# Kernel optimization log

Hardware: AMD Instinct MI355X
Metric: run time of the kernel (lower is better)

## Reference

```python
import jax, jax.numpy as jnp
import numpy as np

NW, NT = 200000, 100000
DW, DT = 128, 64
HID, HEADS, OUT = 64, 2, 2
HC = HID * HEADS  # 128
E = 500000
NEG_SLOPE = 0.2


def setup_inputs() -> dict:
    key = jax.random.key(0)
    ks = iter(jax.random.split(key, 40))

    def nrm(shape, scale):
        return jax.random.normal(next(ks), shape, dtype=jnp.float32) * scale

    inp = {
        "x_wallet": nrm((NW, DW), 1.0),
        "x_token": nrm((NT, DT), 1.0),
        # per-node-type input projections Linear(in, hidden)
        "lin_w_W": nrm((DW, HID), 1.0 / np.sqrt(DW)),
        "lin_w_b": jnp.zeros((HID,), jnp.float32),
        "lin_t_W": nrm((DT, HID), 1.0 / np.sqrt(DT)),
        "lin_t_b": jnp.zeros((HID,), jnp.float32),
        # GAT layer 0: in=HID(64) -> H*C(128), stacked over 3 edge types
        "Wsrc0": nrm((3, HID, HC), 1.0 / np.sqrt(HID)),
        "Wdst0": nrm((3, HID, HC), 1.0 / np.sqrt(HID)),
        "atts0": nrm((3, HEADS, HID), 1.0 / np.sqrt(HID)),
        "attd0": nrm((3, HEADS, HID), 1.0 / np.sqrt(HID)),
        "b0": jnp.zeros((3, HC), jnp.float32),
        # GAT layer 1: in=H*C(128) -> H*C(128)
        "Wsrc1": nrm((3, HC, HC), 1.0 / np.sqrt(HC)),
        "Wdst1": nrm((3, HC, HC), 1.0 / np.sqrt(HC)),
        "atts1": nrm((3, HEADS, HID), 1.0 / np.sqrt(HID)),
        "attd1": nrm((3, HEADS, HID), 1.0 / np.sqrt(HID)),
        "b1": jnp.zeros((3, HC), jnp.float32),
        # classifiers Linear(H*C, out)
        "cls_w_W": nrm((HC, OUT), 1.0 / np.sqrt(HC)),
        "cls_w_b": jnp.zeros((OUT,), jnp.float32),
        "cls_t_W": nrm((HC, OUT), 1.0 / np.sqrt(HC)),
        "cls_t_b": jnp.zeros((OUT,), jnp.float32),
        # edge indices: [2, E] with row0 = src ids, row1 = dst ids
        "e_wt": jnp.stack([jax.random.randint(next(ks), (E,), 0, NW),
                            jax.random.randint(next(ks), (E,), 0, NT)]).astype(jnp.int64),
        "e_tw": jnp.stack([jax.random.randint(next(ks), (E,), 0, NT),
                            jax.random.randint(next(ks), (E,), 0, NW)]).astype(jnp.int64),
        "e_ww": jnp.stack([jax.random.randint(next(ks), (E,), 0, NW),
                            jax.random.randint(next(ks), (E,), 0, NW)]).astype(jnp.int64),
    }
    return inp


def gat_conv(x_src, x_dst, edge, Wsrc, Wdst, att_s, att_d, bias, n_dst):
    # bipartite GATConv: project, per-edge attention, segment softmax over dst, scatter-sum
    hs = (x_src @ Wsrc).reshape(-1, HEADS, HID)  # [Ns,H,C]
    hd = (x_dst @ Wdst).reshape(-1, HEADS, HID)  # [Nd,H,C]
    a_s = jnp.einsum("nhc,hc->nh", hs, att_s)    # [Ns,H]
    a_d = jnp.einsum("nhc,hc->nh", hd, att_d)    # [Nd,H]
    s, d = edge[0], edge[1]
    alpha = jax.nn.leaky_relu(a_s[s] + a_d[d], NEG_SLOPE)  # [E,H]
    m = jax.ops.segment_max(alpha, d, num_segments=n_dst)
    m = jnp.where(jnp.isfinite(m), m, 0.0)  # nodes with no in-edges
    ex = jnp.exp(alpha - m[d])
    den = jax.ops.segment_sum(ex, d, num_segments=n_dst)
    alpha = ex / (den[d] + 1e-16)
    out = jax.ops.segment_sum(alpha[:, :, None] * hs[s], d, num_segments=n_dst)  # [Nd,H,C]
    return out.reshape(n_dst, HC) + bias


def reference(x_wallet, x_token, lin_w_W, lin_w_b, lin_t_W, lin_t_b,
              Wsrc0, Wdst0, atts0, attd0, b0,
              Wsrc1, Wdst1, atts1, attd1, b1,
              cls_w_W, cls_w_b, cls_t_W, cls_t_b,
              e_wt, e_tw, e_ww):
    xw = x_wallet @ lin_w_W + lin_w_b
    xt = x_token @ lin_t_W + lin_t_b
    for Wsrc, Wdst, ats, atd, b in ((Wsrc0, Wdst0, atts0, attd0, b0),
                                     (Wsrc1, Wdst1, atts1, attd1, b1)):
        # edge type 0: wallet->token, 1: token->wallet, 2: wallet->wallet; HeteroConv aggr='sum'
        out_t = gat_conv(xw, xt, e_wt, Wsrc[0], Wdst[0], ats[0], atd[0], b[0], NT)
        out_w = (gat_conv(xt, xw, e_tw, Wsrc[1], Wdst[1], ats[1], atd[1], b[1], NW)
                 + gat_conv(xw, xw, e_ww, Wsrc[2], Wdst[2], ats[2], atd[2], b[2], NW))
        xw = jax.nn.elu(out_w)
        xt = jax.nn.elu(out_t)
    logits_w = xw @ cls_w_W + cls_w_b  # [NW,2]
    logits_t = xt @ cls_t_W + cls_t_b  # [NT,2]
    return jnp.concatenate([logits_w, logits_t], axis=0)  # [NW+NT,2]
```

## Files before the change

kernel.cpp:

```cpp
#include <hip/hip_runtime.h>
#include <stdint.h>

typedef unsigned short ushort_t;
typedef short s8v __attribute__((ext_vector_type(8)));
typedef float f4v __attribute__((ext_vector_type(4)));

#define NW 200000
#define NT 100000
#define EE 500000
#define NSEG (NT + NW + NW)

__device__ __forceinline__ float b2f(unsigned short u){
  union { unsigned int i; float f; } v; v.i = ((unsigned int)u) << 16; return v.f;
}
__device__ __forceinline__ unsigned short f2b(float f){
  unsigned int x = __float_as_uint(f);
  unsigned int r = x + 0x7fffu + ((x >> 16) & 1u);
  return (unsigned short)(r >> 16);
}
__device__ __forceinline__ float ldf(const void* p, long idx, int fm){
  return fm ? ((const float*)p)[idx] : b2f(((const ushort_t*)p)[idx]);
}

__global__ void detect_kern(const int* ewt, const int* etw, const int* eww,
                            const unsigned* xw_words, int* mode){
  if (threadIdx.x == 0 && blockIdx.x == 0){
    unsigned o = 0;
    for (int i = 0; i < 64; ++i)
      o |= (unsigned)ewt[2 * i + 1] | (unsigned)etw[2 * i + 1] | (unsigned)eww[2 * i + 1];
    mode[0] = (o == 0) ? 1 : 0;
    int viol = 0;
    for (int i = 0; i < 256; ++i){
      unsigned s = xw_words[i] & 0xffffu;
      unsigned e = (s >> 7) & 0xffu;
      if (!(s == 0u || s == 0x8000u || (e >= 90u && e <= 140u))) viol++;
    }
    mode[1] = (viol > 8) ? 1 : 0;
  }
}

struct TDesc { const void* src; ushort_t* dst; long ebase; int K; int N; };
struct TDesc8 { TDesc d[8]; };
__global__ void transpose8(TDesc8 td, const int* mode){
  int fm = mode[1];
  int mi = blockIdx.x >> 6;
  TDesc t = td.d[mi];
  int e = ((blockIdx.x & 63) << 8) + threadIdx.x;
  if (e < t.K * t.N){
    int k = e / t.N, n = e - k * t.N;
    t.dst[n * t.K + k] = f2b(ldf(t.src, t.ebase + e, fm));
  }
}

__global__ void uprep(const void* Wsrc0, const void* Wdst0, const void* atts0, const void* attd0,
                      const void* Wsrc1, const void* Wdst1, const void* atts1, const void* attd1,
                      float* Uw0, float* Ut0, float* Uw1, float* Ut1, const int* mode){
  int fm = mode[1];
  int id = blockIdx.x * 256 + threadIdx.x;
  if (id >= (64 + 128) * 12) return;
  int layer = (id >= 64 * 12);
  int rem = layer ? id - 64 * 12 : id;
  int K = layer ? 128 : 64;
  int k = rem / 12, j = rem % 12;
  const void* Ws = layer ? Wsrc1 : Wsrc0;
  const void* Wd = layer ? Wdst1 : Wdst0;
  const void* As = layer ? atts1 : atts0;
  const void* Ad = layer ? attd1 : attd0;
  int t, h; bool src;
  if (j < 8){ const int tt[8] = {0,0,2,2,1,1,2,2}; t = tt[j]; h = j & 1; src = (j < 4); }
  else { int jj = j - 8; t = (jj < 2) ? 1 : 0; h = jj & 1; src = (jj < 2); }
  const void* W = src ? Ws : Wd;
  const void* A = src ? As : Ad;
  float acc = 0.f;
  for (int c = 0; c < 64; ++c)
    acc += ldf(W, (long)(t * K + k) * 128 + h * 64 + c, fm) * ldf(A, t * 128 + h * 64 + c, fm);
  if (j < 8) (layer ? Uw1 : Uw0)[k * 8 + j] = acc;
  else       (layer ? Ut1 : Ut0)[k * 4 + (j - 8)] = acc;
}

__global__ void hist_kern(const int* ewt, const int* etw, const int* eww, const int* mode, int* deg){
  int i = blockIdx.x * 256 + threadIdx.x;
  if (i >= 3 * EE) return;
  int md = mode[0];
  int t = i / EE, e = i - t * EE;
  const int* ep = (t == 0) ? ewt : (t == 1) ? etw : eww;
  int d = md ? ep[2 * (EE + e)] : ep[EE + e];
  int base = (t == 0) ? 0 : (t == 1) ? NT : NT + NW;
  atomicAdd(&deg[base + d], 1);
}

__global__ __launch_bounds__(512) void scan1(const int* deg, int* excl, int* sums){
  __shared__ int pair[512];
  int t = threadIdx.x;
  int base = blockIdx.x * 1024;
  int i0 = base + 2 * t;
  int a = (i0 < NSEG) ? deg[i0] : 0;
  int b = (i0 + 1 < NSEG) ? deg[i0 + 1] : 0;
  int ps = a + b;
  pair[t] = ps;
  __syncthreads();
  for (int off = 1; off < 512; off <<= 1){
    int v = (t >= off) ? pair[t - off] : 0;
    __syncthreads();
    if (t >= off) pair[t] += v;
    __syncthreads();
  }
  int epair = pair[t] - ps;
  if (i0 < NSEG) excl[i0] = epair;
  if (i0 + 1 < NSEG) excl[i0 + 1] = epair + a;
  if (t == 511) sums[blockIdx.x] = pair[511];
}

__global__ __launch_bounds__(512) void scan2(int* sums, int nch){
  __shared__ int s[512];
  int t = threadIdx.x;
  int orig = (t < nch) ? sums[t] : 0;
  s[t] = orig;
  __syncthreads();
  for (int off = 1; off < 512; off <<= 1){
    int v = (t >= off) ? s[t - off] : 0;
    __syncthreads();
    if (t >= off) s[t] += v;
    __syncthreads();
  }
  if (t < nch) sums[t] = s[t] - orig;
}

__global__ void scan3(int* rowptr, int* cursor, const int* sums){
  int i = blockIdx.x * 256 + threadIdx.x;
  if (i < NSEG){
    int v = rowptr[i] + sums[i >> 10];
    rowptr[i] = v; cursor[i] = v;
  }
  if (i == 0) rowptr[NSEG] = 3 * EE;
}

__global__ void fill_kern(const int* ewt, const int* etw, const int* eww, const int* mode,
                          int* cursor, int* adj){
  int i = blockIdx.x * 256 + threadIdx.x;
  if (i >= 3 * EE) return;
  int md = mode[0];
  int t = i / EE, e = i - t * EE;
  const int* ep = (t == 0) ? ewt : (t == 1) ? etw : eww;
  int s = md ? ep[2 * e] : ep[e];
  int d = md ? ep[2 * (EE + e)] : ep[EE + e];
  int base = (t == 0) ? 0 : (t == 1) ? NT : NT + NW;
  int pos = atomicAdd(&cursor[base + d], 1);
  adj[pos] = s;
}

template<int K, int NC, int RS, bool BIAS, bool EXTA>
__global__ __launch_bounds__(256, 2) void gemm_kern(const void* __restrict__ A, const ushort_t* __restrict__ Bt,
    const void* __restrict__ bias, ushort_t* __restrict__ C, int M,
    const int* __restrict__ mode, int nchunk){
  constexpr int CT = NC / 16, KK = K / 32;
  int fm = EXTA ? mode[1] : 0;
  int tid = threadIdx.x, lane = tid & 63, wave = tid >> 6;
  int rl = lane & 15, kq = (lane >> 4) * 8;
  s8v bfrag[CT][KK];
#pragma unroll
  for (int ct = 0; ct < CT; ++ct)
#pragma unroll
    for (int kk = 0; kk < KK; ++kk)
      bfrag[ct][kk] = *(const s8v*)(Bt + (long)(ct * 16 + rl) * K + kk * 32 + kq);
  float biasv[CT];
  if (BIAS){
#pragma unroll
    for (int ct = 0; ct < CT; ++ct) biasv[ct] = ldf(bias, ct * 16 + rl, fm);
  }
  for (int chunk = blockIdx.x; chunk < nchunk; chunk += gridDim.x){
    long m0 = (long)chunk * 128 + wave * 32;
    f4v acc[2][CT];
#pragma unroll
    for (int rt = 0; rt < 2; ++rt)
#pragma unroll
      for (int ct = 0; ct < CT; ++ct) acc[rt][ct] = (f4v){0.f, 0.f, 0.f, 0.f};
#pragma unroll
    for (int rt = 0; rt < 2; ++rt){
      long row = m0 + rt * 16 + rl;
      bool ok = row < (long)M;
#pragma unroll
      for (int kk = 0; kk < KK; ++kk){
        s8v a = (s8v){0,0,0,0,0,0,0,0};
        if (ok){
          long e = row * K + kk * 32 + kq;
          if (EXTA && fm){
            const float* p = (const float*)A + e;
            uint4 lo = *(const uint4*)p;
            uint4 hi = *(const uint4*)(p + 4);
            union { s8v v; unsigned u[4]; } t;
            t.u[0] = (unsigned)f2b(__uint_as_float(lo.x)) | ((unsigned)f2b(__uint_as_float(lo.y)) << 16);
            t.u[1] = (unsigned)f2b(__uint_as_float(lo.z)) | ((unsigned)f2b(__uint_as_float(lo.w)) << 16);
            t.u[2] = (unsigned)f2b(__uint_as_float(hi.x)) | ((unsigned)f2b(__uint_as_float(hi.y)) << 16);
            t.u[3] = (unsigned)f2b(__uint_as_float(hi.z)) | ((unsigned)f2b(__uint_as_float(hi.w)) << 16);
            a = t.v;
          } else {
            a = *(const s8v*)((const ushort_t*)A + e);
          }
        }
#pragma unroll
        for (int ct = 0; ct < CT; ++ct)
          acc[rt][ct] = __builtin_amdgcn_mfma_f32_16x16x32_bf16(a, bfrag[ct][kk], acc[rt][ct], 0, 0, 0);
      }
    }
#pragma unroll
    for (int rt = 0; rt < 2; ++rt){
      long rbase = (long)chunk * 128 + wave * 32 + rt * 16 + (lane >> 4) * 4;
#pragma unroll
      for (int ct = 0; ct < CT; ++ct){
#pragma unroll
        for (int r = 0; r < 4; ++r){
          long gm = rbase + r;
          if (gm < (long)M){
            float v = acc[rt][ct][r];
            if (BIAS) v += biasv[ct];
            C[gm * RS + ct * 16 + rl] = f2b(v);
          }
        }
      }
    }
  }
}

template<int K, bool WAL>
__global__ __launch_bounds__(256) void a_kern(const ushort_t* __restrict__ x, const float* __restrict__ U,
    float* __restrict__ dpq, float* __restrict__ spqA, float* __restrict__ spqB, int N){
  constexpr int NCOL = WAL ? 8 : 4;
  int n = blockIdx.x * 256 + threadIdx.x;
  if (n >= N) return;
  float acc[NCOL];
#pragma unroll
  for (int j = 0; j < NCOL; ++j) acc[j] = 0.f;
  const ushort_t* xr = x + (long)n * K;
#pragma unroll
  for (int k8 = 0; k8 < K / 8; ++k8){
    uint4 v = *(const uint4*)(xr + k8 * 8);
    unsigned uu[4] = {v.x, v.y, v.z, v.w};
#pragma unroll
    for (int i = 0; i < 4; ++i){
      float f0 = b2f((unsigned short)(uu[i] & 0xffffu));
      float f1 = b2f((unsigned short)(uu[i] >> 16));
      const float* Ur = U + (k8 * 8 + i * 2) * NCOL;
#pragma unroll
      for (int j = 0; j < NCOL; ++j) acc[j] += f0 * Ur[j] + f1 * Ur[NCOL + j];
    }
  }
  if (WAL){
    f4v tA = {__expf(acc[0]), __expf(0.2f * acc[0]), __expf(acc[1]), __expf(0.2f * acc[1])};
    *(f4v*)(spqA + (long)n * 4) = tA;
    f4v tB = {__expf(acc[2]), __expf(0.2f * acc[2]), __expf(acc[3]), __expf(0.2f * acc[3])};
    *(f4v*)(spqB + (long)n * 4) = tB;
    f4v d1 = {__expf(acc[4]), __expf(0.2f * acc[4]), __expf(acc[5]), __expf(0.2f * acc[5])};
    f4v d2 = {__expf(acc[6]), __expf(0.2f * acc[6]), __expf(acc[7]), __expf(0.2f * acc[7])};
    *(f4v*)(dpq + (long)n * 8) = d1;
    *(f4v*)(dpq + (long)n * 8 + 4) = d2;
  } else {
    f4v tA = {__expf(acc[0]), __expf(0.2f * acc[0]), __expf(acc[1]), __expf(0.2f * acc[1])};
    *(f4v*)(spqA + (long)n * 4) = tA;
    f4v d0 = {__expf(acc[2]), __expf(0.2f * acc[2]), __expf(acc[3]), __expf(0.2f * acc[3])};
    *(f4v*)(dpq + (long)n * 4) = d0;
  }
}

__device__ __forceinline__ void round_load(const int* __restrict__ adj, int j, int cnt,
    const ushort_t* __restrict__ hs, const float* __restrict__ spq, int c0, int hh,
    float2 (&pq)[8], unsigned (&h)[8]){
#pragma unroll
  for (int i = 0; i < 8; ++i){
    if (i < cnt){
      int s = adj[j + i];
      pq[i] = *(const float2*)(spq + s * 4 + hh * 2);
      h[i] = *(const unsigned*)(hs + (long)s * 128 + c0);
    }
  }
}

__device__ __forceinline__ void round_acc(int cnt, float pd, float qd,
    const float2 (&pq)[8], const unsigned (&h)[8], float& n0, float& n1, float& den){
#pragma unroll
  for (int i = 0; i < 8; ++i){
    if (i < cnt){
      float t = pq[i].x * pd, u = pq[i].y * qd;
      float w = t > 1.f ? t : u;
      den += w;
      n0 += w * b2f((unsigned short)(h[i] & 0xffffu));
      n1 += w * b2f((unsigned short)(h[i] >> 16));
    }
  }
}

__device__ __forceinline__ void classify_store(float o0, float o1, const void* W, const void* b,
    int lane, long g, void* dout, int fm){
  float w00 = ldf(W, 4 * lane + 0, fm), w01 = ldf(W, 4 * lane + 1, fm);
  float w10 = ldf(W, 4 * lane + 2, fm), w11 = ldf(W, 4 * lane + 3, fm);
  float p0 = o0 * w00 + o1 * w10;
  float p1 = o0 * w01 + o1 * w11;
#pragma unroll
  for (int off = 32; off > 0; off >>= 1){ p0 += __shfl_xor(p0, off, 64); p1 += __shfl_xor(p1, off, 64); }
  if (lane == 0){
    float r0 = p0 + ldf(b, 0, fm);
    float r1 = p1 + ldf(b, 1, fm);
    if (fm){ ((float*)dout)[g * 2] = r0; ((float*)dout)[g * 2 + 1] = r1; }
    else { ((ushort_t*)dout)[g * 2] = f2b(r0); ((ushort_t*)dout)[g * 2 + 1] = f2b(r1); }
  }
}

template<bool FINAL>
__global__ __launch_bounds__(256) void agg_tok(const int* __restrict__ rowptr, const int* __restrict__ adj,
    const float* __restrict__ atd, const float* __restrict__ spq0, const ushort_t* __restrict__ hs0,
    const void* __restrict__ bsrc, ushort_t* __restrict__ xt_out,
    const void* __restrict__ clsWt, const void* __restrict__ clsbt,
    void* __restrict__ dout, const int* __restrict__ mode){
  int fm = mode[1];
  int wv = __builtin_amdgcn_readfirstlane(threadIdx.x >> 6);
  int lane = threadIdx.x & 63;
  int hh = lane >> 5, c0 = lane << 1;
  int d = blockIdx.x * 4 + wv;
  float2 dq = *(const float2*)(atd + (long)d * 4 + hh * 2);
  int beg = rowptr[d], end = rowptr[d + 1];
  float n0 = 0.f, n1 = 0.f, den = 0.f;
  for (int j = beg; j < end; j += 8){
    int cnt = min(end - j, 8);
    float2 pq[8]; unsigned h[8];
    round_load(adj, j, cnt, hs0, spq0, c0, hh, pq, h);
    round_acc(cnt, dq.x, dq.y, pq, h, n0, n1, den);
  }
  float inv = 1.f / (den + 1e-16f);
  float o0 = n0 * inv + ldf(bsrc, c0, fm);
  float o1 = n1 * inv + ldf(bsrc, c0 + 1, fm);
  o0 = o0 > 0.f ? o0 : __expf(o0) - 1.f;
  o1 = o1 > 0.f ? o1 : __expf(o1) - 1.f;
  if (!FINAL){
    unsigned pack = (unsigned)f2b(o0) | ((unsigned)f2b(o1) << 16);
    *(unsigned*)(xt_out + (long)d * 128 + c0) = pack;
  } else {
    classify_store(o0, o1, clsWt, clsbt, lane, (long)NW + d, dout, fm);
  }
}

template<bool FINAL>
__global__ __launch_bounds__(256) void agg_wal(const int* __restrict__ rowptr, const int* __restrict__ adj,
    const float* __restrict__ awd, const float* __restrict__ spq1, const float* __restrict__ spq2,
    const ushort_t* __restrict__ hs1, const ushort_t* __restrict__ hs2,
    const void* __restrict__ bsrc, ushort_t* __restrict__ xw_out,
    const void* __restrict__ clsWw, const void* __restrict__ clsbw,
    void* __restrict__ dout, const int* __restrict__ mode){
  int fm = mode[1];
  int wv = __builtin_amdgcn_readfirstlane(threadIdx.x >> 6);
  int lane = threadIdx.x & 63;
  int hh = lane >> 5, c0 = lane << 1;
  int d = blockIdx.x * 4 + wv;
  float2 dq1 = *(const float2*)(awd + (long)d * 8 + hh * 2);
  float2 dq2 = *(const float2*)(awd + (long)d * 8 + 4 + hh * 2);
  int s1 = NT + d, s2 = NT + NW + d;
  int b1 = rowptr[s1], e1 = rowptr[s1 + 1];
  int b2 = rowptr[s2], e2 = rowptr[s2 + 1];
  int c1 = min(e1 - b1, 8), c2 = min(e2 - b2, 8);
  float n10 = 0.f, n11 = 0.f, den1 = 0.f;
  float n20 = 0.f, n21 = 0.f, den2 = 0.f;
  {
    float2 pq1[8], pq2[8]; unsigned h1[8], h2[8];
    if (c1 > 0) round_load(adj, b1, c1, hs1, spq1, c0, hh, pq1, h1);
    if (c2 > 0) round_load(adj, b2, c2, hs2, spq2, c0, hh, pq2, h2);
    if (c1 > 0) round_acc(c1, dq1.x, dq1.y, pq1, h1, n10, n11, den1);
    if (c2 > 0) round_acc(c2, dq2.x, dq2.y, pq2, h2, n20, n21, den2);
  }
  for (int j = b1 + 8; j < e1; j += 8){
    int cnt = min(e1 - j, 8);
    float2 pq[8]; unsigned h[8];
    round_load(adj, j, cnt, hs1, spq1, c0, hh, pq, h);
    round_acc(cnt, dq1.x, dq1.y, pq, h, n10, n11, den1);
  }
  for (int j = b2 + 8; j < e2; j += 8){
    int cnt = min(e2 - j, 8);
    float2 pq[8]; unsigned h[8];
    round_load(adj, j, cnt, hs2, spq2, c0, hh, pq, h);
    round_acc(cnt, dq2.x, dq2.y, pq, h, n20, n21, den2);
  }
  float i1v = 1.f / (den1 + 1e-16f), i2v = 1.f / (den2 + 1e-16f);
  float o0 = n10 * i1v + n20 * i2v + ldf(bsrc, 128 + c0, fm)     + ldf(bsrc, 256 + c0, fm);
  float o1 = n11 * i1v + n21 * i2v + ldf(bsrc, 128 + c0 + 1, fm) + ldf(bsrc, 256 + c0 + 1, fm);
  o0 = o0 > 0.f ? o0 : __expf(o0) - 1.f;
  o1 = o1 > 0.f ? o1 : __expf(o1) - 1.f;
  if (!FINAL){
    unsigned pack = (unsigned)f2b(o0) | ((unsigned)f2b(o1) << 16);
    *(unsigned*)(xw_out + (long)d * 128 + c0) = pack;
  } else {
    classify_store(o0, o1, clsWw, clsbw, lane, (long)d, dout, fm);
  }
}

extern "C" void kernel_launch(void* const* d_in, const int* in_sizes, int n_in,
                              void* d_out, int out_size, void* d_ws, size_t ws_size,
                              hipStream_t stream){
  const void* x_wallet = d_in[0];
  const void* x_token  = d_in[1];
  const void* lin_w_W  = d_in[2];
  const void* lin_w_b  = d_in[3];
  const void* lin_t_W  = d_in[4];
  const void* lin_t_b  = d_in[5];
  const void* Wsrc0    = d_in[6];
  const void* Wdst0    = d_in[7];
  const void* atts0    = d_in[8];
  const void* attd0    = d_in[9];
  const void* b0       = d_in[10];
  const void* Wsrc1    = d_in[11];
  const void* Wdst1    = d_in[12];
  const void* atts1    = d_in[13];
  const void* attd1    = d_in[14];
  const void* b1       = d_in[15];
  const void* cls_w_W  = d_in[16];
  const void* cls_w_b  = d_in[17];
  const void* cls_t_W  = d_in[18];
  const void* cls_t_b  = d_in[19];
  const int* e_wt = (const int*)d_in[20];
  const int* e_tw = (const int*)d_in[21];
  const int* e_ww = (const int*)d_in[22];

  char* ws = (char*)d_ws;
  size_t off = 0;
  auto alloc = [&](size_t bytes) -> char* {
    char* p = ws + off; off += (bytes + 255) & ~(size_t)255; return p;
  };
  int* rowptr = (int*)alloc((size_t)(NSEG + 1) * 4);
  int* deg    = (int*)alloc((size_t)(NSEG + 1) * 4);
  int* adj    = (int*)alloc((size_t)3 * EE * 4);
  int* sums   = (int*)alloc(512 * 4);
  int* mode   = (int*)alloc(8);
  ushort_t* BtLw = (ushort_t*)alloc(64 * 128 * 2);
  ushort_t* BtLt = (ushort_t*)alloc(64 * 64 * 2);
  ushort_t* BtS0 = (ushort_t*)alloc(3 * 128 * 64 * 2);
  ushort_t* BtS1 = (ushort_t*)alloc(3 * 128 * 128 * 2);
  float* Uw0 = (float*)alloc(64 * 8 * 4);
  float* Ut0 = (float*)alloc(64 * 4 * 4);
  float* Uw1 = (float*)alloc(128 * 8 * 4);
  float* Ut1 = (float*)alloc(128 * 4 * 4);
  float* awd = (float*)alloc((size_t)NW * 8 * 4);
  float* atd = (float*)alloc((size_t)NT * 4 * 4);
  float* spq0 = (float*)alloc((size_t)NW * 4 * 4);
  float* spq1 = (float*)alloc((size_t)NT * 4 * 4);
  float* spq2 = (float*)alloc((size_t)NW * 4 * 4);
  ushort_t* hs0 = (ushort_t*)alloc((size_t)NW * 128 * 2);
  ushort_t* hs1 = (ushort_t*)alloc((size_t)NT * 128 * 2);
  ushort_t* hs2 = (ushort_t*)alloc((size_t)NW * 128 * 2);
  ushort_t* xbuf = (ushort_t*)alloc(((size_t)NW + NT) * 128 * 2);
  ushort_t* xw0 = xbuf;
  ushort_t* xt0 = xbuf + (size_t)NW * 64;
  ushort_t* xwB = xbuf;
  ushort_t* xtB = xbuf + (size_t)NW * 128;
  (void)in_sizes; (void)n_in;

  if (off > ws_size){
    hipMemsetAsync(d_out, 0, (size_t)out_size * 2, stream);
    return;
  }

  hipMemsetAsync(deg, 0, (size_t)NSEG * 4, stream);
  detect_kern<<<1, 64, 0, stream>>>(e_wt, e_tw, e_ww, (const unsigned*)x_wallet, mode);

  TDesc8 td;
  td.d[0] = { lin_w_W, BtLw, 0, 128, 64 };
  td.d[1] = { lin_t_W, BtLt, 0, 64, 64 };
  for (int t = 0; t < 3; ++t){
    td.d[2 + t] = { Wsrc0, BtS0 + t * 128 * 64,  (long)t * 64 * 128,  64,  128 };
    td.d[5 + t] = { Wsrc1, BtS1 + t * 128 * 128, (long)t * 128 * 128, 128, 128 };
  }
  transpose8<<<512, 256, 0, stream>>>(td, mode);
  uprep<<<9, 256, 0, stream>>>(Wsrc0, Wdst0, atts0, attd0, Wsrc1, Wdst1, atts1, attd1, Uw0, Ut0, Uw1, Ut1, mode);

  int egrid = (3 * EE + 255) / 256;
  hist_kern<<<egrid, 256, 0, stream>>>(e_wt, e_tw, e_ww, mode, deg);
  int nch = (NSEG + 1023) / 1024;
  scan1<<<nch, 512, 0, stream>>>(deg, rowptr, sums);
  scan2<<<1, 512, 0, stream>>>(sums, nch);
  scan3<<<(NSEG + 255) / 256, 256, 0, stream>>>(rowptr, deg, sums);
  fill_kern<<<egrid, 256, 0, stream>>>(e_wt, e_tw, e_ww, mode, deg, adj);

  const int G = 512;
  int ncW = (NW + 127) / 128, ncT = (NT + 127) / 128;
  int tgrid = NT / 4, wgrid = NW / 4;

  gemm_kern<128, 64, 64, true, true><<<G, 256, 0, stream>>>(x_wallet, BtLw, lin_w_b, xw0, NW, mode, ncW);
  gemm_kern<64, 64, 64, true, true><<<G, 256, 0, stream>>>(x_token, BtLt, lin_t_b, xt0, NT, mode, ncT);

  a_kern<64, true><<<(NW + 255) / 256, 256, 0, stream>>>(xw0, Uw0, awd, spq0, spq2, NW);
  a_kern<64, false><<<(NT + 255) / 256, 256, 0, stream>>>(xt0, Ut0, atd, spq1, nullptr, NT);
  gemm_kern<64, 128, 128, false, false><<<G, 256, 0, stream>>>(xw0, BtS0, nullptr, hs0, NW, mode, ncW);
  agg_tok<false><<<tgrid, 256, 0, stream>>>(rowptr, adj, atd, spq0, hs0, b0, xtB, nullptr, nullptr, nullptr, mode);
  gemm_kern<64, 128, 128, false, false><<<G, 256, 0, stream>>>(xt0, BtS0 + 128 * 64, nullptr, hs1, NT, mode, ncT);
  gemm_kern<64, 128, 128, false, false><<<G, 256, 0, stream>>>(xw0, BtS0 + 2 * 128 * 64, nullptr, hs2, NW, mode, ncW);
  agg_wal<false><<<wgrid, 256, 0, stream>>>(rowptr, adj, awd, spq1, spq2, hs1, hs2, b0, xwB,
                                            nullptr, nullptr, nullptr, mode);

  a_kern<128, true><<<(NW + 255) / 256, 256, 0, stream>>>(xwB, Uw1, awd, spq0, spq2, NW);
  a_kern<128, false><<<(NT + 255) / 256, 256, 0, stream>>>(xtB, Ut1, atd, spq1, nullptr, NT);
  gemm_kern<128, 128, 128, false, false><<<G, 256, 0, stream>>>(xwB, BtS1, nullptr, hs0, NW, mode, ncW);
  agg_tok<true><<<tgrid, 256, 0, stream>>>(rowptr, adj, atd, spq0, hs0, b1, nullptr, cls_t_W, cls_t_b, d_out, mode);
  gemm_kern<128, 128, 128, false, false><<<G, 256, 0, stream>>>(xtB, BtS1 + 128 * 128, nullptr, hs1, NT, mode, ncT);
  gemm_kern<128, 128, 128, false, false><<<G, 256, 0, stream>>>(xwB, BtS1 + 2 * 128 * 128, nullptr, hs2, NW, mode, ncW);
  agg_wal<true><<<wgrid, 256, 0, stream>>>(rowptr, adj, awd, spq1, spq2, hs1, hs2, b1, nullptr,
                                           cls_w_W, cls_w_b, d_out, mode);
}
```

Measured before the change: 910.0 us.

## Merge independent kernels into block-partitioned fused launches to cut launch gaps

Turns the transpose, uprep, hist, fill, GEMM, attention-projection and aggregation kernels into device bodies. Independent work is grouped into combined kernels that split blocks by index range: transpose+uprep, input GEMMs+histogram, layer-0 hs0 GEMM+CSR fill+attention scores, and so on. This removes many serial launch boundaries and lets unrelated stages run concurrently on the GPU. The cost is that merged kernels share launch bounds and register allocation. Heterogeneous blocks can also load-balance unevenly, and the GEMMs now use fixed grid strides of 512, 256 and 384.

New measurement: 891.9 us. 2.0% less time.

```diff
diff --git a/kernel.cpp b/kernel.cpp
--- a/kernel.cpp
+++ b/kernel.cpp
@@ -9,6 +9,12 @@
 #define NT 100000
 #define EE 500000
 #define NSEG (NT + NW + NW)
+
+constexpr int EGRID = (3 * EE + 255) / 256;
+constexpr int AWG   = (NW + 255) / 256;
+constexpr int ATG   = (NT + 255) / 256;
+constexpr int TGRID = NT / 4;
+constexpr int WGRID = NW / 4;
 
 __device__ __forceinline__ float b2f(unsigned short u){
   union { unsigned int i; float f; } v; v.i = ((unsigned int)u) << 16; return v.f;
@@ -41,22 +47,19 @@
 
 struct TDesc { const void* src; ushort_t* dst; long ebase; int K; int N; };
 struct TDesc8 { TDesc d[8]; };
-__global__ void transpose8(TDesc8 td, const int* mode){
-  int fm = mode[1];
-  int mi = blockIdx.x >> 6;
+__device__ __forceinline__ void transpose_body(const TDesc8& td, int fm, int b){
+  int mi = b >> 6;
   TDesc t = td.d[mi];
-  int e = ((blockIdx.x & 63) << 8) + threadIdx.x;
+  int e = ((b & 63) << 8) + threadIdx.x;
   if (e < t.K * t.N){
     int k = e / t.N, n = e - k * t.N;
     t.dst[n * t.K + k] = f2b(ldf(t.src, t.ebase + e, fm));
   }
 }
 
-__global__ void uprep(const void* Wsrc0, const void* Wdst0, const void* atts0, const void* attd0,
-                      const void* Wsrc1, const void* Wdst1, const void* atts1, const void* attd1,
-                      float* Uw0, float* Ut0, float* Uw1, float* Ut1, const int* mode){
-  int fm = mode[1];
-  int id = blockIdx.x * 256 + threadIdx.x;
+__device__ __forceinline__ void uprep_body(const void* Wsrc0, const void* Wdst0, const void* atts0,
+    const void* attd0, const void* Wsrc1, const void* Wdst1, const void* atts1, const void* attd1,
+    float* Uw0, float* Ut0, float* Uw1, float* Ut1, int fm, int id){
   if (id >= (64 + 128) * 12) return;
   int layer = (id >= 64 * 12);
   int rem = layer ? id - 64 * 12 : id;
@@ -78,15 +81,26 @@
   else       (layer ? Ut1 : Ut0)[k * 4 + (j - 8)] = acc;
 }
 
-__global__ void hist_kern(const int* ewt, const int* etw, const int* eww, const int* mode, int* deg){
-  int i = blockIdx.x * 256 + threadIdx.x;
+__device__ __forceinline__ void hist_body(const int* ewt, const int* etw, const int* eww,
+    int md, int* deg, int i){
   if (i >= 3 * EE) return;
-  int md = mode[0];
   int t = i / EE, e = i - t * EE;
   const int* ep = (t == 0) ? ewt : (t == 1) ? etw : eww;
   int d = md ? ep[2 * (EE + e)] : ep[EE + e];
   int base = (t == 0) ? 0 : (t == 1) ? NT : NT + NW;
   atomicAdd(&deg[base + d], 1);
+}
+
+__device__ __forceinline__ void fill_body(const int* ewt, const int* etw, const int* eww,
+    int md, int* cursor, int* adj, int i){
+  if (i >= 3 * EE) return;
+  int t = i / EE, e = i - t * EE;
+  const int* ep = (t == 0) ? ewt : (t == 1) ? etw : eww;
+  int s = md ? ep[2 * e] : ep[e];
+  int d = md ? ep[2 * (EE + e)] : ep[EE + e];
+  int base = (t == 0) ? 0 : (t == 1) ? NT : NT + NW;
+  int pos = atomicAdd(&cursor[base + d], 1);
+  adj[pos] = s;
 }
 
 __global__ __launch_bounds__(512) void scan1(const int* deg, int* excl, int* sums){
@@ -135,26 +149,11 @@
   if (i == 0) rowptr[NSEG] = 3 * EE;
 }
 
-__global__ void fill_kern(const int* ewt, const int* etw, const int* eww, const int* mode,
-                          int* cursor, int* adj){
-  int i = blockIdx.x * 256 + threadIdx.x;
-  if (i >= 3 * EE) return;
-  int md = mode[0];
-  int t = i / EE, e = i - t * EE;
-  const int* ep = (t == 0) ? ewt : (t == 1) ? etw : eww;
-  int s = md ? ep[2 * e] : ep[e];
-  int d = md ? ep[2 * (EE + e)] : ep[EE + e];
-  int base = (t == 0) ? 0 : (t == 1) ? NT : NT + NW;
-  int pos = atomicAdd(&cursor[base + d], 1);
-  adj[pos] = s;
-}
-
 template<int K, int NC, int RS, bool BIAS, bool EXTA>
-__global__ __launch_bounds__(256, 2) void gemm_kern(const void* __restrict__ A, const ushort_t* __restrict__ Bt,
-    const void* __restrict__ bias, ushort_t* __restrict__ C, int M,
-    const int* __restrict__ mode, int nchunk){
+__device__ __forceinline__ void gemm_body(const void* __restrict__ A, const ushort_t* __restrict__ Bt,
+    const void* __restrict__ bias, ushort_t* __restrict__ C, int M, int fm, int nchunk,
+    int bid, int gstr){
   constexpr int CT = NC / 16, KK = K / 32;
-  int fm = EXTA ? mode[1] : 0;
   int tid = threadIdx.x, lane = tid & 63, wave = tid >> 6;
   int rl = lane & 15, kq = (lane >> 4) * 8;
   s8v bfrag[CT][KK];
@@ -168,7 +167,7 @@
 #pragma unroll
     for (int ct = 0; ct < CT; ++ct) biasv[ct] = ldf(bias, ct * 16 + rl, fm);
   }
-  for (int chunk = blockIdx.x; chunk < nchunk; chunk += gridDim.x){
+  for (int chunk = bid; chunk < nchunk; chunk += gstr){
     long m0 = (long)chunk * 128 + wave * 32;
     f4v acc[2][CT];
 #pragma unroll
@@ -223,10 +222,9 @@
 }
 
 template<int K, bool WAL>
-__global__ __launch_bounds__(256) void a_kern(const ushort_t* __restrict__ x, const float* __restrict__ U,
-    float* __restrict__ dpq, float* __restrict__ spqA, float* __restrict__ spqB, int N){
+__device__ __forceinline__ void a_body(const ushort_t* __restrict__ x, const float* __restrict__ U,
+    float* __restrict__ dpq, float* __restrict__ spqA, float* __restrict__ spqB, int N, int n){
   constexpr int NCOL = WAL ? 8 : 4;
-  int n = blockIdx.x * 256 + threadIdx.x;
   if (n >= N) return;
   float acc[NCOL];
 #pragma unroll
@@ -306,16 +304,15 @@
 }
 
 template<bool FINAL>
-__global__ __launch_bounds__(256) void agg_tok(const int* __restrict__ rowptr, const int* __restrict__ adj,
+__device__ __forceinline__ void agg_tok_body(const int* __restrict__ rowptr, const int* __restrict__ adj,
     const float* __restrict__ atd, const float* __restrict__ spq0, const ushort_t* __restrict__ hs0,
     const void* __restrict__ bsrc, ushort_t* __restrict__ xt_out,
     const void* __restrict__ clsWt, const void* __restrict__ clsbt,
-    void* __restrict__ dout, const int* __restrict__ mode){
-  int fm = mode[1];
+    void* __restrict__ dout, int fm, int db){
   int wv = __builtin_amdgcn_readfirstlane(threadIdx.x >> 6);
   int lane = threadIdx.x & 63;
   int hh = lane >> 5, c0 = lane << 1;
-  int d = blockIdx.x * 4 + wv;
+  int d = db * 4 + wv;
   float2 dq = *(const float2*)(atd + (long)d * 4 + hh * 2);
   int beg = rowptr[d], end = rowptr[d + 1];
   float n0 = 0.f, n1 = 0.f, den = 0.f;
@@ -388,6 +385,87 @@
   } else {
     classify_store(o0, o1, clsWw, clsbw, lane, (long)d, dout, fm);
   }
+}
+
+
+__global__ __launch_bounds__(256) void k_tu(TDesc8 td,
+    const void* Wsrc0, const void* Wdst0, const void* atts0, const void* attd0,
+    const void* Wsrc1, const void* Wdst1, const void* atts1, const void* attd1,
+    float* Uw0, float* Ut0, float* Uw1, float* Ut1, const int* mode){
+  int b = blockIdx.x, fm = mode[1];
+  if (b < 512){ transpose_body(td, fm, b); return; }
+  uprep_body(Wsrc0, Wdst0, atts0, attd0, Wsrc1, Wdst1, atts1, attd1,
+             Uw0, Ut0, Uw1, Ut1, fm, (b - 512) * 256 + (int)threadIdx.x);
+}
+
+__global__ __launch_bounds__(256, 2) void k_pre(
+    const void* xw_in, const ushort_t* BtLw, const void* lwb, ushort_t* xw0,
+    const void* xt_in, const ushort_t* BtLt, const void* ltb, ushort_t* xt0,
+    const int* ewt, const int* etw, const int* eww, int* deg,
+    const int* mode, int ncW, int ncT){
+  int b = blockIdx.x;
+  if (b < 512){ gemm_body<128, 64, 64, true, true>(xw_in, BtLw, lwb, xw0, NW, mode[1], ncW, b, 512); return; }
+  b -= 512;
+  if (b < 256){ gemm_body<64, 64, 64, true, true>(xt_in, BtLt, ltb, xt0, NT, mode[1], ncT, b, 256); return; }
+  b -= 256;
+  hist_body(ewt, etw, eww, mode[0], deg, b * 256 + (int)threadIdx.x);
+}
+
+__global__ __launch_bounds__(256, 2) void k_fill(
+    const ushort_t* xw0, const ushort_t* xt0, const ushort_t* BtS0w, ushort_t* hs0,
+    const float* Uw0, const float* Ut0, float* awd, float* atd,
+    float* spq0, float* spq1, float* spq2,
+    const int* ewt, const int* etw, const int* eww, int* cursor, int* adj,
+    const int* mode, int ncW){
+  int b = blockIdx.x;
+  if (b < 512){ gemm_body<64, 128, 128, false, false>(xw0, BtS0w, nullptr, hs0, NW, 0, ncW, b, 512); return; }
+  b -= 512;
+  if (b < EGRID){ fill_body(ewt, etw, eww, mode[0], cursor, adj, b * 256 + (int)threadIdx.x); return; }
+  b -= EGRID;
+  if (b < AWG){ a_body<64, true>(xw0, Uw0, awd, spq0, spq2, NW, b * 256 + (int)threadIdx.x); return; }
+  b -= AWG;
+  a_body<64, false>(xt0, Ut0, atd, spq1, nullptr, NT, b * 256 + (int)threadIdx.x);
+}
+
+__global__ __launch_bounds__(256, 2) void k_tok0(
+    const ushort_t* xt0, const ushort_t* xw0, const ushort_t* BtS0t, const ushort_t* BtS0w2,
+    ushort_t* hs1, ushort_t* hs2,
+    const int* rowptr, const int* adj, const float* atd, const float* spq0,
+    const ushort_t* hs0, const void* b0, ushort_t* xtB,
+    const int* mode, int ncT, int ncW){
+  int b = blockIdx.x;
+  if (b < 256){ gemm_body<64, 128, 128, false, false>(xt0, BtS0t, nullptr, hs1, NT, 0, ncT, b, 256); return; }
+  b -= 256;
+  if (b < 384){ gemm_body<64, 128, 128, false, false>(xw0, BtS0w2, nullptr, hs2, NW, 0, ncW, b, 384); return; }
+  b -= 384;
+  agg_tok_body<false>(rowptr, adj, atd, spq0, hs0, b0, xtB, nullptr, nullptr, nullptr, mode[1], b);
+}
+
+__global__ __launch_bounds__(256, 2) void k_mid1(
+    const ushort_t* xwB, const ushort_t* xtB, const ushort_t* BtS1w, ushort_t* hs0,
+    const float* Uw1, const float* Ut1, float* awd, float* atd,
+    float* spq0, float* spq1, float* spq2, const int* mode, int ncW){
+  int b = blockIdx.x;
+  if (b < 512){ gemm_body<128, 128, 128, false, false>(xwB, BtS1w, nullptr, hs0, NW, 0, ncW, b, 512); return; }
+  b -= 512;
+  if (b < AWG){ a_body<128, true>(xwB, Uw1, awd, spq0, spq2, NW, b * 256 + (int)threadIdx.x); return; }
+  b -= AWG;
+  a_body<128, false>(xtB, Ut1, atd, spq1, nullptr, NT, b * 256 + (int)threadIdx.x);
+}
+
+__global__ __launch_bounds__(256, 2) void k_tok1(
+    const ushort_t* xtB, const ushort_t* xwB, const ushort_t* BtS1t, const ushort_t* BtS1w2,
+    ushort_t* hs1, ushort_t* hs2, const int* mode, int ncT, int ncW){
+  int b = blockIdx.x;
+  if (b < 256){ gemm_body<128, 128, 128, false, false>(xtB, BtS1t, nullptr, hs1, NT, 0, ncT, b, 256); return; }
+  b -= 256;
+  gemm_body<128, 128, 128, false, false>(xwB, BtS1w2, nullptr, hs2, NW, 0, ncW, b, 384);
+}
+
+__global__ __launch_bounds__(256) void agg_tok_fin(const int* rowptr, const int* adj,
+    const float* atd, const float* spq0, const ushort_t* hs0, const void* b1,
+    const void* clsWt, const void* clsbt, void* dout, const int* mode){
+  agg_tok_body<true>(rowptr, adj, atd, spq0, hs0, b1, nullptr, clsWt, clsbt, dout, mode[1], blockIdx.x);
 }
 
 extern "C" void kernel_launch(void* const* d_in, const int* in_sizes, int n_in,
@@ -465,39 +543,31 @@
     td.d[2 + t] = { Wsrc0, BtS0 + t * 128 * 64,  (long)t * 64 * 128,  64,  128 };
     td.d[5 + t] = { Wsrc1, BtS1 + t * 128 * 128, (long)t * 128 * 128, 128, 128 };
   }
-  transpose8<<<512, 256, 0, stream>>>(td, mode);
-  uprep<<<9, 256, 0, stream>>>(Wsrc0, Wdst0, atts0, attd0, Wsrc1, Wdst1, atts1, attd1, Uw0, Ut0, Uw1, Ut1, mode);
-
-  int egrid = (3 * EE + 255) / 256;
-  hist_kern<<<egrid, 256, 0, stream>>>(e_wt, e_tw, e_ww, mode, deg);
+  int ncW = (NW + 127) / 128, ncT = (NT + 127) / 128;
+
+  k_tu<<<521, 256, 0, stream>>>(td, Wsrc0, Wdst0, atts0, attd0, Wsrc1, Wdst1, atts1, attd1,
+                                Uw0, Ut0, Uw1, Ut1, mode);
+  k_pre<<<512 + 256 + EGRID, 256, 0, stream>>>(x_wallet, BtLw, lin_w_b, xw0,
+                                               x_token, BtLt, lin_t_b, xt0,
+                                               e_wt, e_tw, e_ww, deg, mode, ncW, ncT);
   int nch = (NSEG + 1023) / 1024;
   scan1<<<nch, 512, 0, stream>>>(deg, rowptr, sums);
   scan2<<<1, 512, 0, stream>>>(sums, nch);
   scan3<<<(NSEG + 255) / 256, 256, 0, stream>>>(rowptr, deg, sums);
-  fill_kern<<<egrid, 256, 0, stream>>>(e_wt, e_tw, e_ww, mode, deg, adj);
-
-  const int G = 512;
-  int ncW = (NW + 127) / 128, ncT = (NT + 127) / 128;
-  int tgrid = NT / 4, wgrid = NW / 4;
-
-  gemm_kern<128, 64, 64, true, true><<<G, 256, 0, stream>>>(x_wallet, BtLw, lin_w_b, xw0, NW, mode, ncW);
-  gemm_kern<64, 64, 64, true, true><<<G, 256, 0, stream>>>(x_token, BtLt, lin_t_b, xt0, NT, mode, ncT);
-
-  a_kern<64, true><<<(NW + 255) / 256, 256, 0, stream>>>(xw0, Uw0, awd, spq0, spq2, NW);
-  a_kern<64, false><<<(NT + 255) / 256, 256, 0, stream>>>(xt0, Ut0, atd, spq1, nullptr, NT);
-  gemm_kern<64, 128, 128, false, false><<<G, 256, 0, stream>>>(xw0, BtS0, nullptr, hs0, NW, mode, ncW);
-  agg_tok<false><<<tgrid, 256, 0, stream>>>(rowptr, adj, atd, spq0, hs0, b0, xtB, nullptr, nullptr, nullptr, mode);
-  gemm_kern<64, 128, 128, false, false><<<G, 256, 0, stream>>>(xt0, BtS0 + 128 * 64, nullptr, hs1, NT, mode, ncT);
-  gemm_kern<64, 128, 128, false, false><<<G, 256, 0, stream>>>(xw0, BtS0 + 2 * 128 * 64, nullptr, hs2, NW, mode, ncW);
-  agg_wal<false><<<wgrid, 256, 0, stream>>>(rowptr, adj, awd, spq1, spq2, hs1, hs2, b0, xwB,
+
+  k_fill<<<512 + EGRID + AWG + ATG, 256, 0, stream>>>(xw0, xt0, BtS0, hs0,
+      Uw0, Ut0, awd, atd, spq0, spq1, spq2, e_wt, e_tw, e_ww, deg, adj, mode, ncW);
+  k_tok0<<<256 + 384 + TGRID, 256, 0, stream>>>(xt0, xw0, BtS0 + 128 * 64, BtS0 + 2 * 128 * 64,
+      hs1, hs2, rowptr, adj, atd, spq0, hs0, b0, xtB, mode, ncT, ncW);
+  agg_wal<false><<<WGRID, 256, 0, stream>>>(rowptr, adj, awd, spq1, spq2, hs1, hs2, b0, xwB,
                                             nullptr, nullptr, nullptr, mode);
 
-  a_kern<128, true><<<(NW + 255) / 256, 256, 0, stream>>>(xwB, Uw1, awd, spq0, spq2, NW);
-  a_kern<128, false><<<(NT + 255) / 256, 256, 0, stream>>>(xtB, Ut1, atd, spq1, nullptr, NT);
-  gemm_kern<128, 128, 128, false, false><<<G, 256, 0, stream>>>(xwB, BtS1, nullptr, hs0, NW, mode, ncW);
-  agg_tok<true><<<tgrid, 256, 0, stream>>>(rowptr, adj, atd, spq0, hs0, b1, nullptr, cls_t_W, cls_t_b, d_out, mode);
-  gemm_kern<128, 128, 128, false, false><<<G, 256, 0, stream>>>(xtB, BtS1 + 128 * 128, nullptr, hs1, NT, mode, ncT);
-  gemm_kern<128, 128, 128, false, false><<<G, 256, 0, stream>>>(xwB, BtS1 + 2 * 128 * 128, nullptr, hs2, NW, mode, ncW);
-  agg_wal<true><<<wgrid, 256, 0, stream>>>(rowptr, adj, awd, spq1, spq2, hs1, hs2, b1, nullptr,
+  k_mid1<<<512 + AWG + ATG, 256, 0, stream>>>(xwB, xtB, BtS1, hs0,
+      Uw1, Ut1, awd, atd, spq0, spq1, spq2, mode, ncW);
+  k_tok1<<<256 + 384, 256, 0, stream>>>(xtB, xwB, BtS1 + 128 * 128, BtS1 + 2 * 128 * 128,
+                                        hs1, hs2, mode, ncT, ncW);
+  agg_tok_fin<<<TGRID, 256, 0, stream>>>(rowptr, adj, atd, spq0, hs0, b1,
+                                         cls_t_W, cls_t_b, d_out, mode);
+  agg_wal<true><<<WGRID, 256, 0, stream>>>(rowptr, adj, awd, spq1, spq2, hs1, hs2, b1, nullptr,
                                            cls_w_W, cls_w_b, d_out, mode);
 }
```
